# Performance work log

Hardware: AMD Instinct MI355X
Metric: run time of the kernel (lower is better)

The kernel has to match this reference:

```python
import jax, jax.numpy as jnp
import numpy as np

NUM_CLASSES = 151  # Visual Genome object classes
PRED_DIM = 51      # predicate distribution channels (50 predicates + bg)


def _conv2d(x, w, pad):
    # x: [B, Cin, H, W], w: [Cout, Cin, kh, kw]
    return jax.lax.conv_general_dilated(
        x, w, window_strides=(1, 1), padding=[(pad, pad), (pad, pad)],
        dimension_numbers=("NCHW", "OIHW", "NCHW"))


def setup_inputs() -> dict:
    key = jax.random.key(0)
    ks = jax.random.split(key, 12)
    B, N, D = 64, 80, 4096
    K = D // 4  # 1024
    s = 0.02
    return {
        "encoder_reps": jax.random.normal(ks[0], (B, N, D), jnp.float32),
        "obj_preds": jax.random.randint(ks[1], (B, N), 0, NUM_CLASSES, jnp.int32),
        "freq_table": jax.random.normal(ks[2], (NUM_CLASSES * NUM_CLASSES, PRED_DIM), jnp.float32),
        "W_comp": jax.random.normal(ks[3], (D, K), jnp.float32) * s,
        "W_ou1": jax.random.normal(ks[4], (K, K), jnp.float32) * s,
        "W_ofc": jax.random.normal(ks[5], (K, K), jnp.float32) * s,
        "W_decomp": jax.random.normal(ks[6], (K, D), jnp.float32) * s,
        "conv1": jax.random.normal(ks[7], (10, PRED_DIM, 3, 3), jnp.float32) * s,
        "conv2": jax.random.normal(ks[8], (5, 10, 3, 3), jnp.float32) * s,
        "conv3": jax.random.normal(ks[9], (1, 5, 1, 1), jnp.float32) * s,
    }


def reference(encoder_reps, obj_preds, freq_table, W_comp, W_ou1, W_ofc,
              W_decomp, conv1, conv2, conv3):
    B, N, D = encoder_reps.shape
    # obj_comp: Linear(D, D//4, bias=False) + ReLU
    comp = jax.nn.relu(jnp.einsum("bnd,dk->bnk", encoder_reps, W_comp))  # [B,N,K]
    # ou1: Linear(K, K, bias=False) + ReLU
    obj_u1 = jax.nn.relu(jnp.einsum("bnk,kj->bnj", comp, W_ou1))          # [B,N,K]
    # pairwise product indices -> freq_bias.index_with_labels (subj*C + obj)
    pair_idx = obj_preds[:, :, None] * NUM_CLASSES + obj_preds[:, None, :]  # [B,N,N]
    rel_u1 = freq_table[pair_idx]                                          # [B,N,N,51]
    # adjacency via small conv stack + sigmoid
    x = jnp.transpose(rel_u1, (0, 3, 1, 2))      # [B,51,N,N]
    x = _conv2d(x, conv1, pad=1)                 # [B,10,N,N]
    x = _conv2d(x, conv2, pad=1)                 # [B,5,N,N]
    x = _conv2d(x, conv3, pad=0)                 # [B,1,N,N]
    adj = jax.nn.sigmoid(x[:, 0])                # [B,N,N]
    # normalized Laplacian: D^-1/2 (A + I) D^-1/2
    A_hat = adj + jnp.eye(N, dtype=adj.dtype)[None]
    d = (jnp.sum(A_hat, axis=2) + 1e-5) ** (-0.5)                          # [B,N]
    L_hat = d[:, :, None] * A_hat * d[:, None, :]                          # [B,N,N]
    ofl_u = jnp.einsum("bnm,bmk->bnk", L_hat, obj_u1)                      # [B,N,K]
    # ofc_u + obj_decomp + residual
    u_m = jax.nn.relu(jnp.einsum("bnk,kj->bnj", ofl_u, W_ofc))
    decomp = jax.nn.relu(jnp.einsum("bnk,kd->bnd", u_m, W_decomp))
    return decomp + encoder_reps
```

## Files before the change

kernel.cpp:

```cpp
#include <hip/hip_runtime.h>
#include <hip/hip_bf16.h>
#include <math.h>

typedef __bf16 bf16x8 __attribute__((ext_vector_type(8)));
typedef float floatx4 __attribute__((ext_vector_type(4)));
typedef float float4v __attribute__((ext_vector_type(4)));
typedef float float2v __attribute__((ext_vector_type(2)));
typedef unsigned short ushortx4 __attribute__((ext_vector_type(4)));
typedef unsigned short ushortx8 __attribute__((ext_vector_type(8)));

__device__ __forceinline__ unsigned short f2bf(float f) {
    unsigned int u = __builtin_bit_cast(unsigned int, f);
    u += 0x7FFFu + ((u >> 16) & 1u);
    return (unsigned short)(u >> 16);
}
__device__ __forceinline__ float bf2f(unsigned short h) {
    unsigned int u = ((unsigned int)h) << 16;
    return __builtin_bit_cast(float, u);
}

__device__ __forceinline__ void gload_lds16(const void* g, void* l) {
    __builtin_amdgcn_global_load_lds(
        (const __attribute__((address_space(1))) unsigned int*)g,
        (__attribute__((address_space(3))) unsigned int*)l, 16, 0, 0);
}

__global__ __launch_bounds__(256) void cast_bf16_kernel(
    const float* __restrict__ in, unsigned short* __restrict__ out, long n8)
{
    long i = (long)blockIdx.x * 256 + threadIdx.x;
    long stride = (long)gridDim.x * 256;
    for (; i < n8; i += stride) {
        float4v a = reinterpret_cast<const float4v*>(in)[2 * i];
        float4v b = reinterpret_cast<const float4v*>(in)[2 * i + 1];
        ushortx8 h;
        #pragma unroll
        for (int q = 0; q < 4; ++q) { h[q] = f2bf(a[q]); h[4 + q] = f2bf(b[q]); }
        reinterpret_cast<ushortx8*>(out)[i] = h;
    }
}

__global__ __launch_bounds__(256) void reduce3_kernel(
    const unsigned short* __restrict__ p0, const unsigned short* __restrict__ p1,
    const unsigned short* __restrict__ p2, unsigned short* __restrict__ out,
    long n8)
{
    long i = (long)blockIdx.x * 256 + threadIdx.x;
    long stride = (long)gridDim.x * 256;
    const ushortx8* a0 = reinterpret_cast<const ushortx8*>(p0);
    const ushortx8* a1 = reinterpret_cast<const ushortx8*>(p1);
    const ushortx8* a2 = reinterpret_cast<const ushortx8*>(p2);
    for (; i < n8; i += stride) {
        ushortx8 x = a0[i], y = a1[i], zv = a2[i];
        ushortx8 h;
        #pragma unroll
        for (int q = 0; q < 8; ++q)
            h[q] = f2bf(fmaxf(bf2f(x[q]) + bf2f(y[q]) + bf2f(zv[q]), 0.0f));
        reinterpret_cast<ushortx8*>(out)[i] = h;
    }
}

__global__ __launch_bounds__(256) void prep_kernel(
    const float* __restrict__ w1, const float* __restrict__ w2,
    const float* __restrict__ w3, float* __restrict__ W1e,
    float* __restrict__ w23)
{
    for (int idx = threadIdx.x; idx < 4590; idx += 256) {
        int ci = idx / 90, rem = idx % 90;
        int tap = rem / 10, co = rem % 10;
        int di = tap / 3, dj = tap % 3;
        W1e[idx] = w1[((co * 51 + ci) * 3 + di) * 3 + dj];
    }
    if (threadIdx.x < 90) {
        int tap = threadIdx.x / 10, c10 = threadIdx.x % 10;
        int di = tap / 3, dj = tap % 3;
        float s = 0.f;
        #pragma unroll
        for (int c5 = 0; c5 < 5; ++c5)
            s = fmaf(w3[c5], w2[((c5 * 10 + c10) * 3 + di) * 3 + dj], s);
        w23[threadIdx.x] = s;
    }
}

__global__ __launch_bounds__(256) void fp1_kernel(
    const float* __restrict__ freq, const float* __restrict__ W1e,
    float* __restrict__ Fp1)
{
    __shared__ float W1s[4590];
    for (int idx = threadIdx.x; idx < 4590; idx += 256)
        W1s[idx] = W1e[idx];
    __syncthreads();
    int p = blockIdx.x * 256 + threadIdx.x;
    if (p >= 22801) return;
    float2v acc[45];
    #pragma unroll
    for (int t = 0; t < 45; ++t) { acc[t][0] = 0.f; acc[t][1] = 0.f; }
    const float* fr = freq + (size_t)p * 51;
    for (int ci = 0; ci < 51; ++ci) {
        float v = fr[ci];
        const float2v* wrow = reinterpret_cast<const float2v*>(&W1s[ci * 90]);
        #pragma unroll
        for (int t = 0; t < 45; ++t) {
            float2v w = wrow[t];
            acc[t][0] = fmaf(v, w[0], acc[t][0]);
            acc[t][1] = fmaf(v, w[1], acc[t][1]);
        }
    }
    float2v* out = reinterpret_cast<float2v*>(Fp1 + (size_t)p * 90);
    #pragma unroll
    for (int t = 0; t < 45; ++t) out[t] = acc[t];
}

__global__ __launch_bounds__(320) void gather_kernel(
    const int* __restrict__ preds, const float* __restrict__ Fp1,
    float* __restrict__ h1)
{
    __shared__ int pb[80];
    const int b = blockIdx.y;
    const int tid = threadIdx.x;
    if (tid < 80) pb[tid] = preds[b * 80 + tid];
    __syncthreads();
    const int i = blockIdx.x * 4 + tid / 80;
    const int j = tid % 80;
    float2v acc[5];
    #pragma unroll
    for (int q = 0; q < 5; ++q) { acc[q][0] = 0.f; acc[q][1] = 0.f; }
    #pragma unroll
    for (int di = 0; di < 3; ++di) {
        int ii = i + di - 1;
        if (ii < 0 || ii >= 80) continue;
        int pi = pb[ii] * 151;
        #pragma unroll
        for (int dj = 0; dj < 3; ++dj) {
            int jj = j + dj - 1;
            if (jj < 0 || jj >= 80) continue;
            const float2v* row = reinterpret_cast<const float2v*>(
                Fp1 + (size_t)(pi + pb[jj]) * 90 + (di * 3 + dj) * 10);
            #pragma unroll
            for (int q = 0; q < 5; ++q) {
                float2v v = row[q];
                acc[q][0] += v[0];
                acc[q][1] += v[1];
            }
        }
    }
    float2v* out = reinterpret_cast<float2v*>(
        h1 + ((size_t)b * 6400 + i * 80 + j) * 10);
    #pragma unroll
    for (int q = 0; q < 5; ++q) out[q] = acc[q];
}

__global__ __launch_bounds__(320) void conv23_kernel(
    const float* __restrict__ h1, const float* __restrict__ w23g,
    float* __restrict__ adj)
{
    __shared__ float w23s[90];
    const int tid = threadIdx.x;
    if (tid < 90) w23s[tid] = w23g[tid];
    __syncthreads();
    const int b = blockIdx.y;
    const int i = blockIdx.x * 4 + tid / 80;
    const int j = tid % 80;
    float t = 0.f;
    #pragma unroll
    for (int di = 0; di < 3; ++di) {
        int ii = i + di - 1;
        if (ii < 0 || ii >= 80) continue;
        #pragma unroll
        for (int dj = 0; dj < 3; ++dj) {
            int jj = j + dj - 1;
            if (jj < 0 || jj >= 80) continue;
            const float2v* hp = reinterpret_cast<const float2v*>(
                h1 + ((size_t)b * 6400 + ii * 80 + jj) * 10);
            const float* wp = w23s + (di * 3 + dj) * 10;
            #pragma unroll
            for (int q = 0; q < 5; ++q) {
                float2v v = hp[q];
                t = fmaf(v[0], wp[2 * q], t);
                t = fmaf(v[1], wp[2 * q + 1], t);
            }
        }
    }
    adj[(size_t)b * 6400 + i * 80 + j] = 1.0f / (1.0f + __expf(-t));
}

__global__ __launch_bounds__(128) void degree_kernel(
    const float* __restrict__ adj, float* __restrict__ deg)
{
    int b = blockIdx.x;
    int i = threadIdx.x;
    if (i >= 80) return;
    const float* row = adj + (size_t)b * 6400 + i * 80;
    float s = 1.0f + 1e-5f;
    for (int jj = 0; jj < 80; ++jj) s += row[jj];
    deg[b * 80 + i] = rsqrtf(s);
}

__global__ __launch_bounds__(256) void transpose_cast(
    const float* __restrict__ in, unsigned short* __restrict__ out,
    int R, int C)
{
    __shared__ float t[32][33];
    const int tx = threadIdx.x & 31;
    const int ty = threadIdx.x >> 5;
    const int r0 = blockIdx.y * 32, c0 = blockIdx.x * 32;
    #pragma unroll
    for (int k = 0; k < 4; ++k)
        t[ty + k * 8][tx] = in[(size_t)(r0 + ty + k * 8) * C + c0 + tx];
    __syncthreads();
    #pragma unroll
    for (int k = 0; k < 4; ++k)
        out[(size_t)(c0 + ty + k * 8) * R + r0 + tx] = f2bf(t[tx][ty + k * 8]);
}

template<int MODE>
__global__ __launch_bounds__(512, 1) void gemm8(
    const unsigned short* __restrict__ Ap, const unsigned short* __restrict__ Bt,
    void* __restrict__ Cp, const float* __restrict__ Rp,
    unsigned short* __restrict__ P1, unsigned short* __restrict__ P2,
    int M, int N, int lda, int khA, int khB)
{
    __shared__ __align__(16) unsigned short Al[2][2][8192];
    __shared__ __align__(16) unsigned short Bl[2][2][8192];

    const int tid = threadIdx.x;
    const int bm  = blockIdx.x * 256;
    const int bn  = blockIdx.y * 256;
    const int z   = blockIdx.z;
    const int k0  = z ? (khA + (z - 1) * khB) : 0;
    const int kh  = z ? khB : khA;
    const int nt  = kh >> 6;

    const int w    = tid >> 6;
    const int lane = tid & 63;
    const int wr   = w >> 2;
    const int wc   = w & 3;
    const int lr   = lane & 15;
    const int lo   = lane >> 4;
    const int r3   = lr & 3;
    const int soct = (lo ^ r3) * 8;

    floatx4 acc[8][4];
    #pragma unroll
    for (int i = 0; i < 8; ++i)
        #pragma unroll
        for (int j = 0; j < 4; ++j)
            #pragma unroll
            for (int r = 0; r < 4; ++r) acc[i][j][r] = 0.0f;

    auto stageA = [&](int buf, int ks, int kt) {
        #pragma unroll
        for (int it = 0; it < 2; ++it) {
            int d = tid + it * 512;
            int row = d >> 2, s = d & 3;
            gload_lds16(
                &Ap[(size_t)(bm + row) * lda + kt + ks * 32 + ((s ^ (row & 3)) * 8)],
                &Al[buf][ks][d * 8]);
        }
    };
    auto stageB = [&](int buf, int ks, int kt) {
        #pragma unroll
        for (int it = 0; it < 2; ++it) {
            int d = tid + it * 512;
            int row = d >> 2, s = d & 3;
            gload_lds16(
                &Bt[(size_t)(bn + row) * lda + kt + ks * 32 + ((s ^ (row & 3)) * 8)],
                &Bl[buf][ks][d * 8]);
        }
    };

    stageA(0, 0, k0); stageB(0, 0, k0); stageA(0, 1, k0); stageB(0, 1, k0);

    for (int t = 0; t < nt; ++t) {
        const int cur = t & 1;
        const int nxt = cur ^ 1;
        const int ktn = k0 + ((t + 1) << 6);
        const bool pf = (t + 1 < nt);

        asm volatile("s_waitcnt vmcnt(4)" ::: "memory");
        __builtin_amdgcn_s_barrier();
        __builtin_amdgcn_sched_barrier(0);
        bf16x8 b0[4], af[4];
        #pragma unroll
        for (int n = 0; n < 4; ++n)
            b0[n] = *reinterpret_cast<const bf16x8*>(
                &Bl[cur][0][(wc * 64 + n * 16 + lr) * 32 + soct]);
        #pragma unroll
        for (int m = 0; m < 4; ++m)
            af[m] = *reinterpret_cast<const bf16x8*>(
                &Al[cur][0][(wr * 128 + m * 16 + lr) * 32 + soct]);
        if (pf) stageA(nxt, 0, ktn);
        __builtin_amdgcn_s_setprio(1);
        #pragma unroll
        for (int m = 0; m < 4; ++m)
            #pragma unroll
            for (int n = 0; n < 4; ++n)
                acc[m][n] = __builtin_amdgcn_mfma_f32_16x16x32_bf16(
                    af[m], b0[n], acc[m][n], 0, 0, 0);
        __builtin_amdgcn_s_setprio(0);

        #pragma unroll
        for (int m = 0; m < 4; ++m)
            af[m] = *reinterpret_cast<const bf16x8*>(
                &Al[cur][0][(wr * 128 + (m + 4) * 16 + lr) * 32 + soct]);
        if (pf) stageB(nxt, 0, ktn);
        __builtin_amdgcn_s_setprio(1);
        #pragma unroll
        for (int m = 0; m < 4; ++m)
            #pragma unroll
            for (int n = 0; n < 4; ++n)
                acc[m + 4][n] = __builtin_amdgcn_mfma_f32_16x16x32_bf16(
                    af[m], b0[n], acc[m + 4][n], 0, 0, 0);
        __builtin_amdgcn_s_setprio(0);

        if (pf) { asm volatile("s_waitcnt vmcnt(4)" ::: "memory"); }
        else    { asm volatile("s_waitcnt vmcnt(0)" ::: "memory"); }
        __builtin_amdgcn_s_barrier();
        __builtin_amdgcn_sched_barrier(0);
        #pragma unroll
        for (int n = 0; n < 4; ++n)
            b0[n] = *reinterpret_cast<const bf16x8*>(
                &Bl[cur][1][(wc * 64 + n * 16 + lr) * 32 + soct]);
        #pragma unroll
        for (int m = 0; m < 4; ++m)
            af[m] = *reinterpret_cast<const bf16x8*>(
                &Al[cur][1][(wr * 128 + m * 16 + lr) * 32 + soct]);
        if (pf) stageA(nxt, 1, ktn);
        __builtin_amdgcn_s_setprio(1);
        #pragma unroll
        for (int m = 0; m < 4; ++m)
            #pragma unroll
            for (int n = 0; n < 4; ++n)
                acc[m][n] = __builtin_amdgcn_mfma_f32_16x16x32_bf16(
                    af[m], b0[n], acc[m][n], 0, 0, 0);
        __builtin_amdgcn_s_setprio(0);

        #pragma unroll
        for (int m = 0; m < 4; ++m)
            af[m] = *reinterpret_cast<const bf16x8*>(
                &Al[cur][1][(wr * 128 + (m + 4) * 16 + lr) * 32 + soct]);
        if (pf) stageB(nxt, 1, ktn);
        __builtin_amdgcn_s_setprio(1);
        #pragma unroll
        for (int m = 0; m < 4; ++m)
            #pragma unroll
            for (int n = 0; n < 4; ++n)
                acc[m + 4][n] = __builtin_amdgcn_mfma_f32_16x16x32_bf16(
                    af[m], b0[n], acc[m + 4][n], 0, 0, 0);
        __builtin_amdgcn_s_setprio(0);
    }

    unsigned short* dstp = (MODE == 2)
        ? ((z == 0) ? (unsigned short*)Cp : ((z == 1) ? P1 : P2)) : nullptr;
    #pragma unroll
    for (int mi = 0; mi < 8; ++mi) {
        #pragma unroll
        for (int ni = 0; ni < 4; ++ni) {
            #pragma unroll
            for (int rr = 0; rr < 4; ++rr) {
                int row = bm + wr * 128 + mi * 16 + lo * 4 + rr;
                int col = bn + wc * 64 + ni * 16 + lr;
                size_t off = (size_t)row * N + col;
                if (MODE == 1) {
                    ((float*)Cp)[off] = fmaxf(acc[mi][ni][rr], 0.f) + Rp[off];
                } else {
                    dstp[off] = f2bf(acc[mi][ni][rr]);
                }
            }
        }
    }
}

__global__ __launch_bounds__(256) void gemm_pipe0(
    const unsigned short* __restrict__ Ap, const unsigned short* __restrict__ Bt,
    unsigned short* __restrict__ Cp, int M, int N, int lda)
{
    __shared__ unsigned short Al[2][128 * 32];
    __shared__ unsigned short Bl[2][128 * 32];
    const int tid  = threadIdx.x;
    const int bm   = blockIdx.x * 128;
    const int bn   = blockIdx.y * 128;
    const int wave = tid >> 6;
    const int lane = tid & 63;
    const int wm   = (wave >> 1) * 64;
    const int wn   = (wave & 1) * 64;
    const int lr   = lane & 15;
    const int lk   = (lane >> 4) * 8;
    floatx4 acc[4][4];
    #pragma unroll
    for (int i = 0; i < 4; ++i)
        #pragma unroll
        for (int j = 0; j < 4; ++j)
            #pragma unroll
            for (int r = 0; r < 4; ++r) acc[i][j][r] = 0.0f;
    auto stage = [&](int buf, int kq) {
        #pragma unroll
        for (int it = 0; it < 2; ++it) {
            int idx = tid + it * 256;
            gload_lds16(&Ap[(size_t)(bm + (idx >> 2)) * lda + kq + (idx & 3) * 8],
                        &Al[buf][idx * 8]);
        }
        #pragma unroll
        for (int it = 0; it < 2; ++it) {
            int idx = tid + it * 256;
            gload_lds16(&Bt[(size_t)(bn + (idx >> 2)) * lda + kq + (idx & 3) * 8],
                        &Bl[buf][idx * 8]);
        }
    };
    stage(0, 0);
    __syncthreads();
    const int nt = lda >> 5;
    int cur = 0;
    for (int t = 0; t < nt; ++t) {
        if (t + 1 < nt) stage(cur ^ 1, (t + 1) << 5);
        bf16x8 af[4], bfv[4];
        #pragma unroll
        for (int mi = 0; mi < 4; ++mi)
            af[mi] = *reinterpret_cast<const bf16x8*>(
                &Al[cur][(wm + mi * 16 + lr) * 32 + lk]);
        #pragma unroll
        for (int ni = 0; ni < 4; ++ni)
            bfv[ni] = *reinterpret_cast<const bf16x8*>(
                &Bl[cur][(wn + ni * 16 + lr) * 32 + lk]);
        #pragma unroll
        for (int mi = 0; mi < 4; ++mi)
            #pragma unroll
            for (int ni = 0; ni < 4; ++ni)
                acc[mi][ni] = __builtin_amdgcn_mfma_f32_16x16x32_bf16(
                    af[mi], bfv[ni], acc[mi][ni], 0, 0, 0);
        __syncthreads();
        cur ^= 1;
    }
    #pragma unroll
    for (int mi = 0; mi < 4; ++mi)
        #pragma unroll
        for (int ni = 0; ni < 4; ++ni)
            #pragma unroll
            for (int r = 0; r < 4; ++r) {
                int row = bm + wm + mi * 16 + (lane >> 4) * 4 + r;
                int col = bn + wn + ni * 16 + lr;
                Cp[(size_t)row * N + col] = f2bf(fmaxf(acc[mi][ni][r], 0.f));
            }
}

__global__ __launch_bounds__(256) void gemm_f32a(
    const float* __restrict__ Ap, const unsigned short* __restrict__ Bt,
    unsigned short* __restrict__ Cp, int M, int N, int lda)
{
    __shared__ unsigned short Al[2][128 * 40];
    __shared__ unsigned short Bl[2][128 * 32];
    const int tid  = threadIdx.x;
    const int bm   = blockIdx.x * 128;
    const int bn   = blockIdx.y * 128;
    const int wave = tid >> 6;
    const int lane = tid & 63;
    const int wm   = (wave >> 1) * 64;
    const int wn   = (wave & 1) * 64;
    const int lr   = lane & 15;
    const int lk   = (lane >> 4) * 8;
    floatx4 acc[4][4];
    #pragma unroll
    for (int i = 0; i < 4; ++i)
        #pragma unroll
        for (int j = 0; j < 4; ++j)
            #pragma unroll
            for (int r = 0; r < 4; ++r) acc[i][j][r] = 0.0f;
    auto stage = [&](int buf, int k0) {
        #pragma unroll
        for (int it = 0; it < 4; ++it) {
            int idx = tid + it * 256;
            int r = idx >> 3, kc = (idx & 7) * 4;
            float4v v = *reinterpret_cast<const float4v*>(
                &Ap[(size_t)(bm + r) * lda + k0 + kc]);
            ushortx4 h;
            #pragma unroll
            for (int q = 0; q < 4; ++q) h[q] = f2bf(v[q]);
            *reinterpret_cast<ushortx4*>(&Al[buf][r * 40 + kc]) = h;
        }
        #pragma unroll
        for (int it = 0; it < 2; ++it) {
            int idx = tid + it * 256;
            gload_lds16(&Bt[(size_t)(bn + (idx >> 2)) * lda + k0 + (idx & 3) * 8],
                        &Bl[buf][idx * 8]);
        }
    };
    stage(0, 0);
    __syncthreads();
    const int nt = lda >> 5;
    int cur = 0;
    for (int t = 0; t < nt; ++t) {
        if (t + 1 < nt) stage(cur ^ 1, (t + 1) << 5);
        bf16x8 af[4], bfv[4];
        #pragma unroll
        for (int mi = 0; mi < 4; ++mi)
            af[mi] = *reinterpret_cast<const bf16x8*>(
                &Al[cur][(wm + mi * 16 + lr) * 40 + lk]);
        #pragma unroll
        for (int ni = 0; ni < 4; ++ni)
            bfv[ni] = *reinterpret_cast<const bf16x8*>(
                &Bl[cur][(wn + ni * 16 + lr) * 32 + lk]);
        #pragma unroll
        for (int mi = 0; mi < 4; ++mi)
            #pragma unroll
            for (int ni = 0; ni < 4; ++ni)
                acc[mi][ni] = __builtin_amdgcn_mfma_f32_16x16x32_bf16(
                    af[mi], bfv[ni], acc[mi][ni], 0, 0, 0);
        __syncthreads();
        cur ^= 1;
    }
    #pragma unroll
    for (int mi = 0; mi < 4; ++mi)
        #pragma unroll
        for (int ni = 0; ni < 4; ++ni)
            #pragma unroll
            for (int r = 0; r < 4; ++r) {
                int row = bm + wm + mi * 16 + (lane >> 4) * 4 + r;
                int col = bn + wn + ni * 16 + lr;
                Cp[(size_t)row * N + col] = f2bf(fmaxf(acc[mi][ni][r], 0.f));
            }
}

__global__ __launch_bounds__(256) void laplacian_kernel(
    const float* __restrict__ adj, const float* __restrict__ deg,
    const unsigned short* __restrict__ u_in, unsigned short* __restrict__ ofl)
{
    __shared__ float wl[6400];
    __shared__ unsigned short ul[80 * 256];
    const int b   = blockIdx.y;
    const int kq  = blockIdx.x;
    const int tid = threadIdx.x;
    const int ko  = tid & 31;
    const int ngrp = tid >> 5;

    const float* ab = adj + (size_t)b * 6400;
    const float* db = deg + b * 80;
    for (int idx = tid; idx < 6400; idx += 256) {
        int n = idx / 80;
        int m = idx - n * 80;
        float w = ab[idx] + (n == m ? 1.0f : 0.0f);
        wl[idx] = w * db[m];
    }
    const unsigned short* ub = u_in + (size_t)b * 80 * 1024 + kq * 256;
    #pragma unroll
    for (int it = 0; it < 10; ++it) {
        int idx = tid + it * 256;
        int m   = idx >> 5;
        int c8  = (idx & 31) * 8;
        *reinterpret_cast<ushortx8*>(&ul[m * 256 + c8]) =
            *reinterpret_cast<const ushortx8*>(&ub[(size_t)m * 1024 + c8]);
    }
    __syncthreads();

    float acc[10][8];
    #pragma unroll
    for (int ni = 0; ni < 10; ++ni)
        #pragma unroll
        for (int q = 0; q < 8; ++q) acc[ni][q] = 0.0f;

    for (int m = 0; m < 80; ++m) {
        ushortx8 uv = *reinterpret_cast<const ushortx8*>(&ul[m * 256 + ko * 8]);
        float uf[8];
        #pragma unroll
        for (int q = 0; q < 8; ++q) uf[q] = bf2f(uv[q]);
        #pragma unroll
        for (int ni = 0; ni < 10; ++ni) {
            float wv = wl[(ngrp * 10 + ni) * 80 + m];
            #pragma unroll
            for (int q = 0; q < 8; ++q)
                acc[ni][q] = fmaf(wv, uf[q], acc[ni][q]);
        }
    }
    #pragma unroll
    for (int ni = 0; ni < 10; ++ni) {
        int n = ngrp * 10 + ni;
        float dn = db[n];
        ushortx8 o;
        #pragma unroll
        for (int q = 0; q < 8; ++q) o[q] = f2bf(acc[ni][q] * dn);
        *reinterpret_cast<ushortx8*>(
            &ofl[((size_t)(b * 80 + n)) * 1024 + kq * 256 + ko * 8]) = o;
    }
}

extern "C" void kernel_launch(void* const* d_in, const int* in_sizes, int n_in,
                              void* d_out, int out_size, void* d_ws, size_t ws_size,
                              hipStream_t stream)
{
    const float* enc   = (const float*)d_in[0];
    const int*   preds = (const int*)d_in[1];
    const float* freq  = (const float*)d_in[2];
    const float* Wc    = (const float*)d_in[3];
    const float* Wou1  = (const float*)d_in[4];
    const float* Wofc  = (const float*)d_in[5];
    const float* Wdec  = (const float*)d_in[6];
    const float* w1    = (const float*)d_in[7];
    const float* w2    = (const float*)d_in[8];
    const float* w3    = (const float*)d_in[9];

    const int M = 5120;
    const size_t SLAB = (size_t)M * 1024;
    unsigned short* comp  = (unsigned short*)d_ws;
    unsigned short* obju  = comp + SLAB;
    unsigned short* r1    = obju + SLAB;
    unsigned short* oflu  = r1;
    float*          h1    = (float*)r1;
    unsigned short* r2    = r1 + 8192000;
    unsigned short* um    = r2;
    float*          Fp1   = (float*)r2;
    unsigned short* Wcb   = r2 + SLAB;
    unsigned short* Wou1b = Wcb + (size_t)1024 * 4096;
    unsigned short* Wofcb = Wou1b + (size_t)1024 * 1024;
    unsigned short* Wdecb = Wofcb + (size_t)1024 * 1024;
    float*          W1e   = (float*)(Wdecb + (size_t)4096 * 1024);
    float*          w23   = W1e + 4590;
    float*          adj   = w23 + 90;
    float*          deg   = adj + (size_t)64 * 6400;
    unsigned short* encb  = (unsigned short*)(deg + 5120);
    const size_t need_bytes =
        ((size_t)(encb - comp) + (size_t)M * 4096) * sizeof(unsigned short);
    const bool use_encb = ws_size >= need_bytes;
    unsigned short* Q0 = encb;
    unsigned short* Q1 = encb + SLAB;
    unsigned short* Q2 = encb + 2 * SLAB;

    prep_kernel<<<1, 256, 0, stream>>>(w1, w2, w3, W1e, w23);
    transpose_cast<<<dim3(32, 128), 256, 0, stream>>>(Wc, Wcb, 4096, 1024);
    transpose_cast<<<dim3(32, 32), 256, 0, stream>>>(Wou1, Wou1b, 1024, 1024);
    transpose_cast<<<dim3(32, 32), 256, 0, stream>>>(Wofc, Wofcb, 1024, 1024);
    transpose_cast<<<dim3(128, 32), 256, 0, stream>>>(Wdec, Wdecb, 1024, 4096);

    fp1_kernel<<<90, 256, 0, stream>>>(freq, W1e, Fp1);
    gather_kernel<<<dim3(20, 64), 320, 0, stream>>>(preds, Fp1, h1);
    conv23_kernel<<<dim3(20, 64), 320, 0, stream>>>(h1, w23, adj);
    degree_kernel<<<64, 128, 0, stream>>>(adj, deg);

    if (use_encb) {
        cast_bf16_kernel<<<2048, 256, 0, stream>>>(enc, encb, (long)M * 4096 / 8);
        gemm8<2><<<dim3(20, 4, 3), 512, 0, stream>>>(
            encb, Wcb, r1, nullptr, r2, obju, M, 1024, 4096, 1408, 1344);
        reduce3_kernel<<<2048, 256, 0, stream>>>(r1, r2, obju, comp, SLAB / 8);
        gemm8<2><<<dim3(20, 4, 3), 512, 0, stream>>>(
            comp, Wou1b, Q0, nullptr, Q1, Q2, M, 1024, 1024, 384, 320);
        reduce3_kernel<<<2048, 256, 0, stream>>>(Q0, Q1, Q2, obju, SLAB / 8);
    } else {
        gemm_f32a<<<dim3(40, 8), 256, 0, stream>>>(enc, Wcb, comp, M, 1024, 4096);
        gemm_pipe0<<<dim3(40, 8), 256, 0, stream>>>(comp, Wou1b, obju, M, 1024, 1024);
    }
    laplacian_kernel<<<dim3(4, 64), 256, 0, stream>>>(adj, deg, obju, oflu);
    if (use_encb) {
        gemm8<2><<<dim3(20, 4, 3), 512, 0, stream>>>(
            oflu, Wofcb, Q0, nullptr, Q1, Q2, M, 1024, 1024, 384, 320);
        reduce3_kernel<<<2048, 256, 0, stream>>>(Q0, Q1, Q2, um, SLAB / 8);
    } else {
        gemm_pipe0<<<dim3(40, 8), 256, 0, stream>>>(oflu, Wofcb, um, M, 1024, 1024);
    }
    gemm8<1><<<dim3(20, 16, 1), 512, 0, stream>>>(
        um, Wdecb, d_out, enc, nullptr, nullptr, M, 4096, 1024, 1024, 0);
}
```

Measured before the change: 331.9 us.

## Stage GEMM epilogue through swizzled LDS for coalesced vector stores

The GEMM epilogue previously wrote each accumulator element as a scalar store with a strided pattern. Now the MFMA operands are swapped so each lane holds four consecutive columns, and the tile is staged through a reused, XOR-swizzled shared-memory buffer. Rows are then written back with 16-byte coalesced stores, and the fp32 residual-add mode reads the residual vectorised in two half-tile passes. This aims to cut uncoalesced global write traffic, at the cost of extra LDS round trips and barriers.

After: 329.3 us. Within noise of the previous version (-0.8%).

```diff
diff --git a/kernel.cpp b/kernel.cpp
--- a/kernel.cpp
+++ b/kernel.cpp
@@ -220,8 +220,9 @@
     unsigned short* __restrict__ P1, unsigned short* __restrict__ P2,
     int M, int N, int lda, int khA, int khB)
 {
-    __shared__ __align__(16) unsigned short Al[2][2][8192];
-    __shared__ __align__(16) unsigned short Bl[2][2][8192];
+    __shared__ __align__(16) unsigned short S[65536];
+    auto Apl = [&](int buf, int ks) { return S + (buf * 2 + ks) * 8192; };
+    auto Bpl = [&](int buf, int ks) { return S + 32768 + (buf * 2 + ks) * 8192; };
 
     const int tid = threadIdx.x;
     const int bm  = blockIdx.x * 256;
@@ -255,7 +256,7 @@
             int row = d >> 2, s = d & 3;
             gload_lds16(
                 &Ap[(size_t)(bm + row) * lda + kt + ks * 32 + ((s ^ (row & 3)) * 8)],
-                &Al[buf][ks][d * 8]);
+                &Apl(buf, ks)[d * 8]);
         }
     };
     auto stageB = [&](int buf, int ks, int kt) {
@@ -265,7 +266,7 @@
             int row = d >> 2, s = d & 3;
             gload_lds16(
                 &Bt[(size_t)(bn + row) * lda + kt + ks * 32 + ((s ^ (row & 3)) * 8)],
-                &Bl[buf][ks][d * 8]);
+                &Bpl(buf, ks)[d * 8]);
         }
     };
 
@@ -284,11 +285,11 @@
         #pragma unroll
         for (int n = 0; n < 4; ++n)
             b0[n] = *reinterpret_cast<const bf16x8*>(
-                &Bl[cur][0][(wc * 64 + n * 16 + lr) * 32 + soct]);
+                &Bpl(cur, 0)[(wc * 64 + n * 16 + lr) * 32 + soct]);
         #pragma unroll
         for (int m = 0; m < 4; ++m)
             af[m] = *reinterpret_cast<const bf16x8*>(
-                &Al[cur][0][(wr * 128 + m * 16 + lr) * 32 + soct]);
+                &Apl(cur, 0)[(wr * 128 + m * 16 + lr) * 32 + soct]);
         if (pf) stageA(nxt, 0, ktn);
         __builtin_amdgcn_s_setprio(1);
         #pragma unroll
@@ -296,13 +297,13 @@
             #pragma unroll
             for (int n = 0; n < 4; ++n)
                 acc[m][n] = __builtin_amdgcn_mfma_f32_16x16x32_bf16(
-                    af[m], b0[n], acc[m][n], 0, 0, 0);
+                    b0[n], af[m], acc[m][n], 0, 0, 0);
         __builtin_amdgcn_s_setprio(0);
 
         #pragma unroll
         for (int m = 0; m < 4; ++m)
             af[m] = *reinterpret_cast<const bf16x8*>(
-                &Al[cur][0][(wr * 128 + (m + 4) * 16 + lr) * 32 + soct]);
+                &Apl(cur, 0)[(wr * 128 + (m + 4) * 16 + lr) * 32 + soct]);
         if (pf) stageB(nxt, 0, ktn);
         __builtin_amdgcn_s_setprio(1);
         #pragma unroll
@@ -310,7 +311,7 @@
             #pragma unroll
             for (int n = 0; n < 4; ++n)
                 acc[m + 4][n] = __builtin_amdgcn_mfma_f32_16x16x32_bf16(
-                    af[m], b0[n], acc[m + 4][n], 0, 0, 0);
+                    b0[n], af[m], acc[m + 4][n], 0, 0, 0);
         __builtin_amdgcn_s_setprio(0);
 
         if (pf) { asm volatile("s_waitcnt vmcnt(4)" ::: "memory"); }
@@ -320,11 +321,11 @@
         #pragma unroll
         for (int n = 0; n < 4; ++n)
             b0[n] = *reinterpret_cast<const bf16x8*>(
-                &Bl[cur][1][(wc * 64 + n * 16 + lr) * 32 + soct]);
+                &Bpl(cur, 1)[(wc * 64 + n * 16 + lr) * 32 + soct]);
         #pragma unroll
         for (int m = 0; m < 4; ++m)
             af[m] = *reinterpret_cast<const bf16x8*>(
-                &Al[cur][1][(wr * 128 + m * 16 + lr) * 32 + soct]);
+                &Apl(cur, 1)[(wr * 128 + m * 16 + lr) * 32 + soct]);
         if (pf) stageA(nxt, 1, ktn);
         __builtin_amdgcn_s_setprio(1);
         #pragma unroll
@@ -332,13 +333,13 @@
             #pragma unroll
             for (int n = 0; n < 4; ++n)
                 acc[m][n] = __builtin_amdgcn_mfma_f32_16x16x32_bf16(
-                    af[m], b0[n], acc[m][n], 0, 0, 0);
+                    b0[n], af[m], acc[m][n], 0, 0, 0);
         __builtin_amdgcn_s_setprio(0);
 
         #pragma unroll
         for (int m = 0; m < 4; ++m)
             af[m] = *reinterpret_cast<const bf16x8*>(
-                &Al[cur][1][(wr * 128 + (m + 4) * 16 + lr) * 32 + soct]);
+                &Apl(cur, 1)[(wr * 128 + (m + 4) * 16 + lr) * 32 + soct]);
         if (pf) stageB(nxt, 1, ktn);
         __builtin_amdgcn_s_setprio(1);
         #pragma unroll
@@ -346,27 +347,74 @@
             #pragma unroll
             for (int n = 0; n < 4; ++n)
                 acc[m + 4][n] = __builtin_amdgcn_mfma_f32_16x16x32_bf16(
-                    af[m], b0[n], acc[m + 4][n], 0, 0, 0);
+                    b0[n], af[m], acc[m + 4][n], 0, 0, 0);
         __builtin_amdgcn_s_setprio(0);
     }
 
-    unsigned short* dstp = (MODE == 2)
-        ? ((z == 0) ? (unsigned short*)Cp : ((z == 1) ? P1 : P2)) : nullptr;
-    #pragma unroll
-    for (int mi = 0; mi < 8; ++mi) {
-        #pragma unroll
-        for (int ni = 0; ni < 4; ++ni) {
-            #pragma unroll
-            for (int rr = 0; rr < 4; ++rr) {
-                int row = bm + wr * 128 + mi * 16 + lo * 4 + rr;
-                int col = bn + wc * 64 + ni * 16 + lr;
-                size_t off = (size_t)row * N + col;
-                if (MODE == 1) {
-                    ((float*)Cp)[off] = fmaxf(acc[mi][ni][rr], 0.f) + Rp[off];
-                } else {
-                    dstp[off] = f2bf(acc[mi][ni][rr]);
+    __syncthreads();
+
+    if (MODE == 2) {
+        #pragma unroll
+        for (int mi = 0; mi < 8; ++mi) {
+            const int mrow = wr * 128 + mi * 16 + lr;
+            const int swz = (mrow & 7) << 4;
+            #pragma unroll
+            for (int ni = 0; ni < 4; ++ni) {
+                const int ncol = wc * 64 + ni * 16 + lo * 4;
+                ushortx4 v;
+                #pragma unroll
+                for (int rr = 0; rr < 4; ++rr) v[rr] = f2bf(acc[mi][ni][rr]);
+                *reinterpret_cast<ushortx4*>(
+                    (char*)S + ((mrow * 512 + ncol * 2) ^ swz)) = v;
+            }
+        }
+        __syncthreads();
+        unsigned short* dst =
+            (z == 0) ? (unsigned short*)Cp : ((z == 1) ? P1 : P2);
+        #pragma unroll
+        for (int it = 0; it < 16; ++it) {
+            int idx = tid + it * 512;
+            int r = idx >> 5, c = idx & 31;
+            ushortx8 v = *reinterpret_cast<const ushortx8*>(
+                (char*)S + ((r * 512 + c * 16) ^ ((r & 7) << 4)));
+            *reinterpret_cast<ushortx8*>(
+                &dst[(size_t)(bm + r) * N + bn + c * 8]) = v;
+        }
+    } else {
+        #pragma unroll
+        for (int p = 0; p < 2; ++p) {
+            if ((wc >> 1) == p) {
+                #pragma unroll
+                for (int mi = 0; mi < 8; ++mi) {
+                    const int mrow = wr * 128 + mi * 16 + lr;
+                    const int swz = (mrow & 7) << 4;
+                    #pragma unroll
+                    for (int ni = 0; ni < 4; ++ni) {
+                        const int nc = (wc & 1) * 64 + ni * 16 + lo * 4;
+                        float4v v;
+                        #pragma unroll
+                        for (int rr = 0; rr < 4; ++rr) v[rr] = acc[mi][ni][rr];
+                        *reinterpret_cast<float4v*>(
+                            (char*)S + ((mrow * 512 + nc * 4) ^ swz)) = v;
+                    }
                 }
             }
+            __syncthreads();
+            #pragma unroll
+            for (int it = 0; it < 16; ++it) {
+                int idx = tid + it * 512;
+                int r = idx >> 5, c = idx & 31;
+                float4v v = *reinterpret_cast<const float4v*>(
+                    (char*)S + ((r * 512 + c * 16) ^ ((r & 7) << 4)));
+                size_t off = (size_t)(bm + r) * N + bn + p * 128 + c * 4;
+                float4v rv = *reinterpret_cast<const float4v*>(&Rp[off]);
+                float4v o;
+                #pragma unroll
+                for (int rr = 0; rr < 4; ++rr)
+                    o[rr] = fmaxf(v[rr], 0.f) + rv[rr];
+                *reinterpret_cast<float4v*>(&((float*)Cp)[off]) = o;
+            }
+            if (p == 0) __syncthreads();
         }
     }
 }
```
